# Optimization experiments

Measured on AMD Instinct MI355X. Metric: run time of the kernel, lower is better.

Reference implementation:

```python
import jax, jax.numpy as jnp
import numpy as np

EPS = 1e-6
BN_EPS = 1e-5
K = 20

def _vn_linear(x, W):
    # x: [B,C,...] channel axis 1; W: [out,in]
    return jnp.einsum('oc,bc...->bo...', W, x)

def _vn_bn(x):
    # training-mode BatchNorm on per-vector norms (affine at init: gamma=1, beta=0)
    norm = jnp.sqrt(jnp.sum(x * x, axis=2)) + EPS  # [B,C,*spatial]
    axes = (0,) + tuple(range(2, norm.ndim))
    mean = jnp.mean(norm, axis=axes, keepdims=True)
    var = jnp.mean((norm - mean) ** 2, axis=axes, keepdims=True)  # biased, as torch BN
    norm_bn = (norm - mean) / jnp.sqrt(var + BN_EPS)
    return x / jnp.expand_dims(norm, 2) * jnp.expand_dims(norm_bn, 2)

def _vn_llr(x, Wf, Wd, ns=0.0, use_bn=True):
    p = _vn_linear(x, Wf)
    if use_bn:
        p = _vn_bn(p)
    d = _vn_linear(x, Wd)
    dot = jnp.sum(p * d, axis=2, keepdims=True)
    mask = (dot >= 0).astype(x.dtype)
    dsq = jnp.sum(d * d, axis=2, keepdims=True)
    return ns * p + (1.0 - ns) * (mask * p + (1.0 - mask) * (p - dot / (dsq + EPS) * d))

def _graph_feature_cross(x, k):
    # x: [B,3,N] -> [B,3,3,N,k]
    B, _, N = x.shape
    inner = -2.0 * jnp.einsum('bdn,bdm->bnm', x, x)
    xx = jnp.sum(x * x, axis=1)  # [B,N]
    pdist = -xx[:, :, None] - inner - xx[:, None, :]  # [B,N,N]
    idx = jax.lax.top_k(pdist, k)[1]  # [B,N,k] nearest neighbors
    xt = jnp.transpose(x, (0, 2, 1))  # [B,N,3]
    nbr = xt[jnp.arange(B)[:, None, None], idx]  # [B,N,k,3]
    ctr = jnp.broadcast_to(xt[:, :, None, :], nbr.shape)  # [B,N,k,3]
    cross = jnp.cross(nbr, ctr)
    feat = jnp.stack([nbr - ctr, ctr, cross], axis=3)  # [B,N,k,3ch,3vec]
    return jnp.transpose(feat, (0, 3, 4, 1, 2))  # [B,3,3,N,k]

def _forward(points, wposf, wposd, w1f, w1d, w2f, w2d, w3, ws1f, ws1d, ws2f, ws2d, wlin):
    x = jnp.transpose(points, (0, 2, 1))  # [B,3,N]
    B, _, N = x.shape
    feat = _graph_feature_cross(x, K)  # [B,3,3,N,K]
    x = _vn_llr(feat, wposf, wposd)  # conv_pos, dim=5 -> [B,21,3,N,K]
    x = jnp.mean(x, axis=-1)  # mean pool over k -> [B,21,3,N]
    x = _vn_llr(x, w1f, w1d)  # conv1
    x = _vn_llr(x, w2f, w2d)  # conv2 (feature_transform=False so in=21? no: conv2 takes 42 -- matches cat-free path only when feature_transform False? conv2 in=42 but code passes x of 21? original passes 21-ch into conv2 only if feature_transform else 21; here feature_transform=False and conv2 expects 42 in torch -- we mirror with w2f [42,42] applied after duplicating? No: mirror exact torch behavior below.)
    return x

def reference(points, wposf, wposd, w1f, w1d, w2f, w2d, w3, ws1f, ws1d, ws2f, ws2d, wlin):
    x = jnp.transpose(points, (0, 2, 1))  # [B,3,N]
    B, _, N = x.shape
    feat = _graph_feature_cross(x, K)  # [B,3,3,N,K]
    x = _vn_llr(feat, wposf, wposd)  # [B,21,3,N,K]
    x = jnp.mean(x, axis=-1)  # mean pool -> [B,21,3,N]
    x = _vn_llr(x, w1f, w1d)  # [B,21,3,N]
    # torch conv2 is Linear(42,42) but with feature_transform=False it is applied to 21-ch
    # input; nn.Linear would error, so faithful runnable form uses the duplicated-channel
    # convention: concat (x, x) is NOT in the original; instead we slice w2 to [42,21].
    x = _vn_llr(x, w2f[:, :21], w2d[:, :21])  # [B,42,3,N]
    x = _vn_bn(_vn_linear(x, w3))  # conv3 + bn3 -> [B,85,3,N]
    x_mean_out = jnp.mean(x, axis=-1, keepdims=True)  # [B,85,3,1]
    x = jnp.concatenate([x, jnp.broadcast_to(x_mean_out, x.shape)], axis=1)  # [B,170,3,N]
    z = _vn_llr(x, ws1f, ws1d)  # [B,85,3,N]
    z = _vn_llr(z, ws2f, ws2d)  # [B,42,3,N]
    z = _vn_linear(z, wlin)  # [B,3,3,N]
    z = jnp.transpose(z, (0, 2, 1, 3))  # [B,3,3,N]
    x_std = jnp.einsum('bijm,bjkm->bikm', x, z)  # [B,170,3,N]
    xf = x_std.reshape(B, -1, N)  # [B,510,N]
    inv_z = jnp.max(xf, axis=-1)  # [B,510]
    center_loc = jnp.mean(x_mean_out, axis=2)  # [B,85,1]
    return (inv_z, x_mean_out, center_loc)

def setup_inputs() -> dict:
    key = jax.random.key(0)
    ks = jax.random.split(key, 14)
    B, N = 4, 8192
    def w(k, shape):
        return (jax.random.normal(k, shape, dtype=jnp.float32) * (1.0 / np.sqrt(shape[1])))
    return {
        'points': jax.random.normal(ks[0], (B, N, 3), dtype=jnp.float32),
        'wposf': w(ks[1], (21, 3)),
        'wposd': w(ks[2], (21, 3)),
        'w1f': w(ks[3], (21, 21)),
        'w1d': w(ks[4], (21, 21)),
        'w2f': w(ks[5], (42, 42)),
        'w2d': w(ks[6], (42, 42)),
        'w3': w(ks[7], (85, 42)),
        'ws1f': w(ks[8], (85, 170)),
        'ws1d': w(ks[9], (85, 170)),
        'ws2f': w(ks[10], (42, 85)),
        'ws2d': w(ks[11], (42, 85)),
        'wlin': w(ks[12], (3, 42)),
    }
```

## Files before the change

kernel.cpp:

```cpp
#include <hip/hip_runtime.h>
#include <cstdint>
#include <cstddef>

#define EPSF 1e-6f
#define BN_EPSF 1e-5f

constexpr int Bb = 4;
constexpr int Nn = 8192;
constexpr int KK = 20;
constexpr int SEG = 8;
constexpr int SEGLEN = Nn / SEG;
constexpr int BUF = 24;

constexpr size_t KNN0_OFF = 0;
constexpr size_t KNN1_OFF = 5242880;
constexpr size_t X1_OFF  = 0;
constexpr size_t X2_OFF  = 2064384;
constexpr size_t X3_OFF  = 4128768;
constexpr size_t Z1_OFF  = 0;
constexpr size_t X4_OFF  = 8355840;
constexpr size_t IDX_OFF = 16711680;
constexpr size_t Z2_OFF  = 17367040;
constexpr size_t Z3_OFF  = 21495808;
constexpr size_t ACC_OFF = 21790720;
constexpr size_t XM_OFF  = 21791744;
constexpr size_t BF_OFF  = 21792764;
constexpr size_t BD_OFF  = 21793784;
constexpr size_t DEXT_OFF = 21795840;
constexpr size_t EXT_NEED = (DEXT_OFF + 8355840) * 4;

__device__ __forceinline__ float wave_sum(float v) {
#pragma unroll
  for (int off = 32; off; off >>= 1) v += __shfl_xor(v, off, 64);
  return v;
}
__device__ __forceinline__ float wave_max(float v) {
#pragma unroll
  for (int off = 32; off; off >>= 1) v = fmaxf(v, __shfl_xor(v, off, 64));
  return v;
}
__device__ __forceinline__ uint32_t umin32(uint32_t a, uint32_t b) { return a < b ? a : b; }
__device__ __forceinline__ uint32_t umax32(uint32_t a, uint32_t b) { return a < b ? b : a; }

__global__ __launch_bounds__(1024) void zero_acc(float* __restrict__ a) {
  a[threadIdx.x] = 0.f;
}

__global__ __launch_bounds__(256) void knn_kernel(const float* __restrict__ pts,
                                                  uint32_t* __restrict__ knnp) {
  __shared__ float4 tile[SEGLEN];
  __shared__ uint32_t buf[BUF * 256];
  const int tid = threadIdx.x;
  const int n = blockIdx.x * 256 + tid;
  const int b = blockIdx.y;
  const int s = blockIdx.z;
  const float* pb = pts + (size_t)b * Nn * 3;

  for (int i = tid; i < SEGLEN; i += 256) {
    const float* p = pb + (size_t)(s * SEGLEN + i) * 3;
    const float x = p[0], y = p[1], z = p[2];
    tile[i] = make_float4(x, y, z, 0.5f * (x * x + y * y + z * z));
  }
  const float qx = pb[n * 3 + 0], qy = pb[n * 3 + 1], qz = pb[n * 3 + 2];
  const float nqx = -qx, nqy = -qy, nqz = -qz;
  const float h = 0.5f * (qx * qx + qy * qy + qz * qz);
  __syncthreads();

  uint32_t keys[KK];
#pragma unroll
  for (int j = 0; j < KK; ++j) keys[j] = 0xFFFFFFFFu;

  const int base = s * SEGLEN;

#pragma unroll 4
  for (int j = 0; j < 64; ++j) {
    const float4 c = tile[j];
    float u = fmaf(nqx, c.x, fmaf(nqy, c.y, fmaf(nqz, c.z, c.w + h)));
    u = fmaxf(u, 0.f);
    uint32_t mx = (__float_as_uint(u) & 0xFFFFE000u) | (uint32_t)(base + j);
#pragma unroll
    for (int q = 0; q < KK; ++q) {
      const uint32_t mn = umin32(keys[q], mx);
      mx = umax32(keys[q], mx);
      keys[q] = mn;
    }
  }

  uint32_t thresh = keys[KK - 1];
  float thresh_up = __uint_as_float((thresh & 0xFFFFE000u) + 0x2000u);
  int cnt = 0;

  for (int j0 = 64; j0 < SEGLEN; j0 += 4) {
#pragma unroll
    for (int u4 = 0; u4 < 4; ++u4) {
      const int j = j0 + u4;
      const float4 c = tile[j];
      const float u = fmaf(nqx, c.x, fmaf(nqy, c.y, fmaf(nqz, c.z, c.w + h)));
      if (u < thresh_up) {
        const float uc = fmaxf(u, 0.f);
        const uint32_t key = (__float_as_uint(uc) & 0xFFFFE000u) | (uint32_t)(base + j);
        buf[cnt * 256 + tid] = key;
        ++cnt;
      }
    }
    if (__any(cnt > BUF - 4)) {
#pragma unroll
      for (int i = 0; i < BUF; ++i) {
        uint32_t mx = (i < cnt) ? buf[i * 256 + tid] : 0xFFFFFFFFu;
#pragma unroll
        for (int q = 0; q < KK; ++q) {
          const uint32_t mn = umin32(keys[q], mx);
          mx = umax32(keys[q], mx);
          keys[q] = mn;
        }
      }
      cnt = 0;
      thresh = keys[KK - 1];
      thresh_up = __uint_as_float((thresh & 0xFFFFE000u) + 0x2000u);
    }
  }
#pragma unroll
  for (int i = 0; i < BUF; ++i) {
    uint32_t mx = (i < cnt) ? buf[i * 256 + tid] : 0xFFFFFFFFu;
#pragma unroll
    for (int q = 0; q < KK; ++q) {
      const uint32_t mn = umin32(keys[q], mx);
      mx = umax32(keys[q], mx);
      keys[q] = mn;
    }
  }

  uint32_t* op = knnp + ((size_t)(b * SEG + s) * KK) * Nn + n;
#pragma unroll
  for (int j = 0; j < KK; ++j) op[(size_t)j * Nn] = keys[j];
}

template <int LIN>
__global__ __launch_bounds__(256) void merge_pass(const uint32_t* __restrict__ in,
                                                  uint32_t* __restrict__ out) {
  constexpr int LOUT = LIN / 2;
  const int t = blockIdx.x * 256 + threadIdx.x;
  const int n = t & (Nn - 1);
  const int r = t >> 13;
  const int j = r % LOUT, b = r / LOUT;
  const uint32_t* p0 = in + ((size_t)(b * LIN + 2 * j) * KK) * Nn + n;
  const uint32_t* p1 = in + ((size_t)(b * LIN + 2 * j + 1) * KK) * Nn + n;
  uint32_t* op = out + ((size_t)(b * LOUT + j) * KK) * Nn + n;
  int i0 = 0, i1 = 0;
  uint32_t k0 = p0[0], k1 = p1[0];
#pragma unroll
  for (int m = 0; m < KK; ++m) {
    uint32_t k;
    if (k0 <= k1) { k = k0; ++i0; k0 = (i0 < KK) ? p0[(size_t)i0 * Nn] : 0xFFFFFFFFu; }
    else          { k = k1; ++i1; k1 = (i1 < KK) ? p1[(size_t)i1 * Nn] : 0xFFFFFFFFu; }
    op[(size_t)m * Nn] = k;
  }
}

__global__ __launch_bounds__(256) void merge_final(const uint32_t* __restrict__ in,
                                                   int* __restrict__ idx) {
  const int t = blockIdx.x * 256 + threadIdx.x;
  const int n = t & (Nn - 1), b = t >> 13;
  const uint32_t* p0 = in + ((size_t)(b * 2 + 0) * KK) * Nn + n;
  const uint32_t* p1 = in + ((size_t)(b * 2 + 1) * KK) * Nn + n;
  int* op = idx + (size_t)t * KK;
  int i0 = 0, i1 = 0;
  uint32_t k0 = p0[0], k1 = p1[0];
#pragma unroll
  for (int m = 0; m < KK; ++m) {
    uint32_t k;
    if (k0 <= k1) { k = k0; ++i0; k0 = (i0 < KK) ? p0[(size_t)i0 * Nn] : 0xFFFFFFFFu; }
    else          { k = k1; ++i1; k1 = (i1 < KK) ? p1[(size_t)i1 * Nn] : 0xFFFFFFFFu; }
    op[m] = (int)(k & 8191u);
  }
}

__global__ __launch_bounds__(256) void s1_stats(const float* __restrict__ pts,
                                                const int* __restrict__ idx,
                                                const float* __restrict__ wf,
                                                float* __restrict__ acc) {
  __shared__ float lacc[42];
  const int tid = threadIdx.x;
  for (int i = tid; i < 42; i += 256) lacc[i] = 0.f;
  __syncthreads();
  const int t = blockIdx.x * 256 + tid;
  const int site = t / 5;
  const int kq = (t % 5) * 4;
  const int n = site & (Nn - 1), b = site >> 13;
  const float* pb = pts + (size_t)b * Nn * 3;
  const float cx = pb[n * 3 + 0], cy = pb[n * 3 + 1], cz = pb[n * 3 + 2];
  float s1a[21], s2a[21];
#pragma unroll
  for (int o = 0; o < 21; ++o) { s1a[o] = 0.f; s2a[o] = 0.f; }
#pragma unroll
  for (int k = kq; k < kq + 4; ++k) {
    const int m = idx[(size_t)site * KK + k];
    const float ax = pb[m * 3 + 0], ay = pb[m * 3 + 1], az = pb[m * 3 + 2];
    const float e0x = ax - cx, e0y = ay - cy, e0z = az - cz;
    const float e2x = ay * cz - az * cy, e2y = az * cx - ax * cz, e2z = ax * cy - ay * cx;
#pragma unroll
    for (int o = 0; o < 21; ++o) {
      const float w0 = wf[o * 3 + 0], w1 = wf[o * 3 + 1], w2 = wf[o * 3 + 2];
      const float px = w0 * e0x + w1 * cx + w2 * e2x;
      const float py = w0 * e0y + w1 * cy + w2 * e2y;
      const float pz = w0 * e0z + w1 * cz + w2 * e2z;
      const float nrm = sqrtf(px * px + py * py + pz * pz) + EPSF;
      s1a[o] += nrm;
      s2a[o] += nrm * nrm;
    }
  }
#pragma unroll
  for (int o = 0; o < 21; ++o) {
    const float s1 = wave_sum(s1a[o]);
    const float s2 = wave_sum(s2a[o]);
    if ((tid & 63) == 0) { atomicAdd(&lacc[o], s1); atomicAdd(&lacc[21 + o], s2); }
  }
  __syncthreads();
  for (int i = tid; i < 42; i += 256) atomicAdd(&acc[i], lacc[i]);
}

__global__ __launch_bounds__(256) void s1_apply(const float* __restrict__ pts,
                                                const int* __restrict__ idx,
                                                const float* __restrict__ wf,
                                                const float* __restrict__ wd,
                                                const float* __restrict__ acc,
                                                float* __restrict__ x1) {
  const int t = blockIdx.x * 256 + threadIdx.x;
  const int o0 = blockIdx.y * 7;
  const int n = t & (Nn - 1), b = t >> 13;
  const float* pb = pts + (size_t)b * Nn * 3;
  const float cx = pb[n * 3 + 0], cy = pb[n * 3 + 1], cz = pb[n * 3 + 2];
  const float inv_cnt = 1.f / (float)(Bb * Nn * KK);
  float meano[7], istdo[7];
#pragma unroll
  for (int j = 0; j < 7; ++j) {
    const float mn = acc[o0 + j] * inv_cnt;
    const float vr = acc[21 + o0 + j] * inv_cnt - mn * mn;
    meano[j] = mn;
    istdo[j] = rsqrtf(vr + BN_EPSF);
  }
  float accu[7][3];
#pragma unroll
  for (int j = 0; j < 7; ++j) { accu[j][0] = 0.f; accu[j][1] = 0.f; accu[j][2] = 0.f; }
  for (int k = 0; k < KK; ++k) {
    const int m = idx[(size_t)t * KK + k];
    const float ax = pb[m * 3 + 0], ay = pb[m * 3 + 1], az = pb[m * 3 + 2];
    const float e0x = ax - cx, e0y = ay - cy, e0z = az - cz;
    const float e2x = ay * cz - az * cy, e2y = az * cx - ax * cz, e2z = ax * cy - ay * cx;
#pragma unroll
    for (int j = 0; j < 7; ++j) {
      const int o = o0 + j;
      const float wf0 = wf[o * 3 + 0], wf1 = wf[o * 3 + 1], wf2 = wf[o * 3 + 2];
      const float px = wf0 * e0x + wf1 * cx + wf2 * e2x;
      const float py = wf0 * e0y + wf1 * cy + wf2 * e2y;
      const float pz = wf0 * e0z + wf1 * cz + wf2 * e2z;
      const float nrm = sqrtf(px * px + py * py + pz * pz) + EPSF;
      const float factor = (nrm - meano[j]) * istdo[j] / nrm;
      const float q0 = px * factor, q1 = py * factor, q2 = pz * factor;
      const float wd0 = wd[o * 3 + 0], wd1 = wd[o * 3 + 1], wd2 = wd[o * 3 + 2];
      const float dx = wd0 * e0x + wd1 * cx + wd2 * e2x;
      const float dy = wd0 * e0y + wd1 * cy + wd2 * e2y;
      const float dz = wd0 * e0z + wd1 * cz + wd2 * e2z;
      const float dot = q0 * dx + q1 * dy + q2 * dz;
      const float dsq = dx * dx + dy * dy + dz * dz;
      const float corr = (dot < 0.f) ? dot / (dsq + EPSF) : 0.f;
      accu[j][0] += q0 - corr * dx;
      accu[j][1] += q1 - corr * dy;
      accu[j][2] += q2 - corr * dz;
    }
  }
  const float sc = 1.f / (float)KK;
  float* ob = x1 + (size_t)b * 21 * 3 * Nn + n;
#pragma unroll
  for (int j = 0; j < 7; ++j) {
    const int o = o0 + j;
    ob[(o * 3 + 0) * Nn] = accu[j][0] * sc;
    ob[(o * 3 + 1) * Nn] = accu[j][1] * sc;
    ob[(o * 3 + 2) * Nn] = accu[j][2] * sc;
  }
}

template <int CIN, int COUT, int OT, bool HAS_BIAS>
__global__ __launch_bounds__(256) void vn_stats_pd(const float* __restrict__ X,
                                                   const float* __restrict__ Wf,
                                                   const float* __restrict__ Wd, int ws,
                                                   const float* __restrict__ biasF,
                                                   const float* __restrict__ biasD,
                                                   float* __restrict__ acc,
                                                   float* __restrict__ P,
                                                   float* __restrict__ D) {
  __shared__ float lacc[2 * OT];
  const int tid = threadIdx.x;
  if (tid < 2 * OT) lacc[tid] = 0.f;
  __syncthreads();
  const int o0 = blockIdx.y * OT;
  const int t = blockIdx.x * 256 + tid;
  const int n = t & (Nn - 1), b = t >> 13;
  const float* xb = X + (size_t)b * CIN * 3 * Nn + n;
  float* pb = P + (size_t)b * COUT * 3 * Nn + n;
  float* db = D + (size_t)b * COUT * 3 * Nn + n;
  float p[OT][3], dv[OT][3];
#pragma unroll
  for (int j = 0; j < OT; ++j)
#pragma unroll
    for (int dd = 0; dd < 3; ++dd) {
      p[j][dd] = HAS_BIAS ? biasF[((size_t)b * COUT + o0 + j) * 3 + dd] : 0.f;
      dv[j][dd] = HAS_BIAS ? biasD[((size_t)b * COUT + o0 + j) * 3 + dd] : 0.f;
    }
  for (int c = 0; c < CIN; ++c) {
    const float x0 = xb[(c * 3 + 0) * Nn];
    const float x1v = xb[(c * 3 + 1) * Nn];
    const float x2v = xb[(c * 3 + 2) * Nn];
#pragma unroll
    for (int j = 0; j < OT; ++j) {
      const float wfv = Wf[(o0 + j) * ws + c];
      p[j][0] += wfv * x0; p[j][1] += wfv * x1v; p[j][2] += wfv * x2v;
      const float wdv = Wd[(o0 + j) * ws + c];
      dv[j][0] += wdv * x0; dv[j][1] += wdv * x1v; dv[j][2] += wdv * x2v;
    }
  }
#pragma unroll
  for (int j = 0; j < OT; ++j) {
    const int o = o0 + j;
    pb[(size_t)(o * 3 + 0) * Nn] = p[j][0];
    pb[(size_t)(o * 3 + 1) * Nn] = p[j][1];
    pb[(size_t)(o * 3 + 2) * Nn] = p[j][2];
    db[(size_t)(o * 3 + 0) * Nn] = dv[j][0];
    db[(size_t)(o * 3 + 1) * Nn] = dv[j][1];
    db[(size_t)(o * 3 + 2) * Nn] = dv[j][2];
  }
#pragma unroll
  for (int j = 0; j < OT; ++j) {
    const float nrm = sqrtf(p[j][0] * p[j][0] + p[j][1] * p[j][1] + p[j][2] * p[j][2]) + EPSF;
    const float s1 = wave_sum(nrm);
    const float s2 = wave_sum(nrm * nrm);
    if ((tid & 63) == 0) { atomicAdd(&lacc[j], s1); atomicAdd(&lacc[OT + j], s2); }
  }
  __syncthreads();
  if (tid < 2 * OT) {
    const int g = (tid < OT) ? (o0 + tid) : (COUT + o0 + (tid - OT));
    atomicAdd(&acc[g], lacc[tid]);
  }
}

__device__ __forceinline__ float llr_one(float p0, float p1, float p2,
                                         float d0, float d1, float d2,
                                         float mn, float istd,
                                         float& r0o, float& r1o, float& r2o) {
  const float nrm = sqrtf(p0 * p0 + p1 * p1 + p2 * p2) + EPSF;
  const float factor = (nrm - mn) * istd / nrm;
  float r0 = p0 * factor, r1 = p1 * factor, r2 = p2 * factor;
  const float dot = r0 * d0 + r1 * d1 + r2 * d2;
  const float dsq = d0 * d0 + d1 * d1 + d2 * d2;
  const float corr = (dot < 0.f) ? dot / (dsq + EPSF) : 0.f;
  r0o = r0 - corr * d0; r1o = r1 - corr * d1; r2o = r2 - corr * d2;
  return 0.f;
}

template <int COUT>
__global__ __launch_bounds__(256) void vn_llr_ew4(const float* __restrict__ acc, float cntinv,
                                                  float* __restrict__ P,
                                                  const float* __restrict__ D) {
  const int t = blockIdx.x * 256 + threadIdx.x;
  const int n4 = t & (Nn / 4 - 1);
  const int r = t >> 11;
  const int o = r % COUT, b = r / COUT;
  float4* pp = (float4*)(P + ((size_t)(b * COUT + o) * 3) * Nn) + n4;
  const float4* dp = (const float4*)(D + ((size_t)(b * COUT + o) * 3) * Nn) + n4;
  const float4 p0 = pp[0], p1 = pp[Nn / 4], p2 = pp[2 * (Nn / 4)];
  const float4 d0 = dp[0], d1 = dp[Nn / 4], d2 = dp[2 * (Nn / 4)];
  const float mn = acc[o] * cntinv;
  const float vr = acc[COUT + o] * cntinv - mn * mn;
  const float istd = rsqrtf(vr + BN_EPSF);
  float4 r0, r1, r2;
  llr_one(p0.x, p1.x, p2.x, d0.x, d1.x, d2.x, mn, istd, r0.x, r1.x, r2.x);
  llr_one(p0.y, p1.y, p2.y, d0.y, d1.y, d2.y, mn, istd, r0.y, r1.y, r2.y);
  llr_one(p0.z, p1.z, p2.z, d0.z, d1.z, d2.z, mn, istd, r0.z, r1.z, r2.z);
  llr_one(p0.w, p1.w, p2.w, d0.w, d1.w, d2.w, mn, istd, r0.w, r1.w, r2.w);
  pp[0] = r0;
  pp[Nn / 4] = r1;
  pp[2 * (Nn / 4)] = r2;
}

template <int CIN, int COUT, int OT, bool HAS_BIAS>
__global__ __launch_bounds__(256) void vn_stats_pc(const float* __restrict__ X,
                                                   const float* __restrict__ Wf, int ws,
                                                   const float* __restrict__ biasF,
                                                   float* __restrict__ acc,
                                                   float* __restrict__ P) {
  __shared__ float lacc[2 * OT];
  const int tid = threadIdx.x;
  if (tid < 2 * OT) lacc[tid] = 0.f;
  __syncthreads();
  const int o0 = blockIdx.y * OT;
  const int t = blockIdx.x * 256 + tid;
  const int n = t & (Nn - 1), b = t >> 13;
  const float* xb = X + (size_t)b * CIN * 3 * Nn + n;
  float* pb = P + (size_t)b * COUT * 3 * Nn + n;
  float p[OT][3];
#pragma unroll
  for (int j = 0; j < OT; ++j)
#pragma unroll
    for (int dd = 0; dd < 3; ++dd)
      p[j][dd] = HAS_BIAS ? biasF[((size_t)b * COUT + o0 + j) * 3 + dd] : 0.f;
  for (int c = 0; c < CIN; ++c) {
    const float x0 = xb[(c * 3 + 0) * Nn];
    const float x1v = xb[(c * 3 + 1) * Nn];
    const float x2v = xb[(c * 3 + 2) * Nn];
#pragma unroll
    for (int j = 0; j < OT; ++j) {
      const float wv = Wf[(o0 + j) * ws + c];
      p[j][0] += wv * x0; p[j][1] += wv * x1v; p[j][2] += wv * x2v;
    }
  }
#pragma unroll
  for (int j = 0; j < OT; ++j) {
    const int o = o0 + j;
    pb[(size_t)(o * 3 + 0) * Nn] = p[j][0];
    pb[(size_t)(o * 3 + 1) * Nn] = p[j][1];
    pb[(size_t)(o * 3 + 2) * Nn] = p[j][2];
  }
#pragma unroll
  for (int j = 0; j < OT; ++j) {
    const float nrm = sqrtf(p[j][0] * p[j][0] + p[j][1] * p[j][1] + p[j][2] * p[j][2]) + EPSF;
    const float s1 = wave_sum(nrm);
    const float s2 = wave_sum(nrm * nrm);
    if ((tid & 63) == 0) { atomicAdd(&lacc[j], s1); atomicAdd(&lacc[OT + j], s2); }
  }
  __syncthreads();
  if (tid < 2 * OT) {
    const int g = (tid < OT) ? (o0 + tid) : (COUT + o0 + (tid - OT));
    atomicAdd(&acc[g], lacc[tid]);
  }
}

template <int CIN, int COUT, int OT, bool HAS_BIAS>
__global__ __launch_bounds__(256) void vn_apply_pc(const float* __restrict__ X,
                                                   const float* __restrict__ Wd, int ws,
                                                   const float* __restrict__ biasD,
                                                   const float* __restrict__ acc, float cntinv,
                                                   float* __restrict__ P) {
  const int o0 = blockIdx.y * OT;
  const int t = blockIdx.x * 256 + threadIdx.x;
  const int n = t & (Nn - 1), b = t >> 13;
  const float* xb = X + (size_t)b * CIN * 3 * Nn + n;
  float* pb = P + (size_t)b * COUT * 3 * Nn + n;
  float dv[OT][3];
#pragma unroll
  for (int j = 0; j < OT; ++j)
#pragma unroll
    for (int dd = 0; dd < 3; ++dd)
      dv[j][dd] = HAS_BIAS ? biasD[((size_t)b * COUT + o0 + j) * 3 + dd] : 0.f;
  for (int c = 0; c < CIN; ++c) {
    const float x0 = xb[(c * 3 + 0) * Nn];
    const float x1v = xb[(c * 3 + 1) * Nn];
    const float x2v = xb[(c * 3 + 2) * Nn];
#pragma unroll
    for (int j = 0; j < OT; ++j) {
      const float wdv = Wd[(o0 + j) * ws + c];
      dv[j][0] += wdv * x0; dv[j][1] += wdv * x1v; dv[j][2] += wdv * x2v;
    }
  }
#pragma unroll
  for (int j = 0; j < OT; ++j) {
    const int o = o0 + j;
    const float p0 = pb[(size_t)(o * 3 + 0) * Nn];
    const float p1 = pb[(size_t)(o * 3 + 1) * Nn];
    const float p2 = pb[(size_t)(o * 3 + 2) * Nn];
    const float nrm = sqrtf(p0 * p0 + p1 * p1 + p2 * p2) + EPSF;
    const float mn = acc[o] * cntinv;
    const float vr = acc[COUT + o] * cntinv - mn * mn;
    const float factor = (nrm - mn) * rsqrtf(vr + BN_EPSF) / nrm;
    float r0 = p0 * factor, r1 = p1 * factor, r2 = p2 * factor;
    const float dot = r0 * dv[j][0] + r1 * dv[j][1] + r2 * dv[j][2];
    const float dsq = dv[j][0] * dv[j][0] + dv[j][1] * dv[j][1] + dv[j][2] * dv[j][2];
    const float corr = (dot < 0.f) ? dot / (dsq + EPSF) : 0.f;
    r0 -= corr * dv[j][0]; r1 -= corr * dv[j][1]; r2 -= corr * dv[j][2];
    pb[(size_t)(o * 3 + 0) * Nn] = r0;
    pb[(size_t)(o * 3 + 1) * Nn] = r1;
    pb[(size_t)(o * 3 + 2) * Nn] = r2;
  }
}

template <int COUT>
__global__ __launch_bounds__(256) void vn_bn4(const float* __restrict__ acc, float cntinv,
                                              float* __restrict__ P) {
  const int t = blockIdx.x * 256 + threadIdx.x;
  const int n4 = t & (Nn / 4 - 1);
  const int r = t >> 11;
  const int o = r % COUT, b = r / COUT;
  float4* pp = (float4*)(P + ((size_t)(b * COUT + o) * 3) * Nn) + n4;
  const float4 p0 = pp[0], p1 = pp[Nn / 4], p2 = pp[2 * (Nn / 4)];
  const float mn = acc[o] * cntinv;
  const float vr = acc[COUT + o] * cntinv - mn * mn;
  const float istd = rsqrtf(vr + BN_EPSF);
  float4 r0, r1, r2;
#define BN_ONE(f) {                                                        \
    const float nrm = sqrtf(p0.f * p0.f + p1.f * p1.f + p2.f * p2.f) + EPSF; \
    const float factor = (nrm - mn) * istd / nrm;                          \
    r0.f = p0.f * factor; r1.f = p1.f * factor; r2.f = p2.f * factor; }
  BN_ONE(x) BN_ONE(y) BN_ONE(z) BN_ONE(w)
#undef BN_ONE
  pp[0] = r0;
  pp[Nn / 4] = r1;
  pp[2 * (Nn / 4)] = r2;
}

__global__ __launch_bounds__(256) void s5_mean(const float* __restrict__ x4,
                                               float* __restrict__ xm,
                                               float* __restrict__ out) {
  const int row = blockIdx.x;
  const int b = row / 255, rcd = row % 255;
  const float* src = x4 + (size_t)b * 255 * Nn + (size_t)rcd * Nn;
  float s = 0.f;
  for (int n = threadIdx.x; n < Nn; n += 256) s += src[n];
  s = wave_sum(s);
  __shared__ float wsum[4];
  if ((threadIdx.x & 63) == 0) wsum[threadIdx.x >> 6] = s;
  __syncthreads();
  if (threadIdx.x == 0) {
    const float mv = (wsum[0] + wsum[1] + wsum[2] + wsum[3]) * (1.f / (float)Nn);
    xm[row] = mv;
    out[2040 + row] = mv;
  }
}

__global__ __launch_bounds__(256) void s5_bias(const float* __restrict__ xm,
                                               const float* __restrict__ ws1f,
                                               const float* __restrict__ ws1d,
                                               float* __restrict__ biasF,
                                               float* __restrict__ biasD,
                                               float* __restrict__ out) {
  const int t = blockIdx.x * 256 + threadIdx.x;
  if (t < 1020) {
    const int b = t / 255, r = t % 255, o = r / 3, dd = r % 3;
    float sf = 0.f, sd = 0.f;
    for (int c = 0; c < 85; ++c) {
      const float xv = xm[(b * 85 + c) * 3 + dd];
      sf += ws1f[o * 170 + 85 + c] * xv;
      sd += ws1d[o * 170 + 85 + c] * xv;
    }
    biasF[t] = sf;
    biasD[t] = sd;
  }
  if (t < 340) {
    const int b = t / 85, c = t % 85;
    out[3060 + t] = (xm[(b * 85 + c) * 3 + 0] + xm[(b * 85 + c) * 3 + 1] +
                     xm[(b * 85 + c) * 3 + 2]) * (1.f / 3.f);
  }
}

__global__ __launch_bounds__(256) void s8_z3(const float* __restrict__ z2,
                                             const float* __restrict__ wlin,
                                             float* __restrict__ z3) {
  const int t = blockIdx.x * 256 + threadIdx.x;
  const int n = t & (Nn - 1), b = t >> 13;
  const float* zb = z2 + (size_t)b * 42 * 3 * Nn + n;
  float accv[3][3];
#pragma unroll
  for (int o = 0; o < 3; ++o)
#pragma unroll
    for (int dd = 0; dd < 3; ++dd) accv[o][dd] = 0.f;
  for (int c = 0; c < 42; ++c) {
    const float x0 = zb[(c * 3 + 0) * Nn];
    const float x1v = zb[(c * 3 + 1) * Nn];
    const float x2v = zb[(c * 3 + 2) * Nn];
#pragma unroll
    for (int o = 0; o < 3; ++o) {
      const float wv = wlin[o * 42 + c];
      accv[o][0] += wv * x0; accv[o][1] += wv * x1v; accv[o][2] += wv * x2v;
    }
  }
  float* ob = z3 + (size_t)b * 9 * Nn + n;
#pragma unroll
  for (int o = 0; o < 3; ++o)
#pragma unroll
    for (int dd = 0; dd < 3; ++dd) ob[(o * 3 + dd) * Nn] = accv[o][dd];
}

__global__ __launch_bounds__(256) void s9_max(const float* __restrict__ x4,
                                              const float* __restrict__ xm,
                                              const float* __restrict__ z3,
                                              float* __restrict__ out) {
  const int tile = blockIdx.x;
  const int b = blockIdx.y;
  const int i0 = tile * 5;
  const bool upper = (i0 >= 85);
  float mx[15];
#pragma unroll
  for (int r = 0; r < 15; ++r) mx[r] = -3.402823466e38f;
  float xmr[5][3];
  if (upper) {
#pragma unroll
    for (int ii = 0; ii < 5; ++ii)
#pragma unroll
      for (int j = 0; j < 3; ++j) xmr[ii][j] = xm[(b * 85 + (i0 - 85 + ii)) * 3 + j];
  }
  const float* zb = z3 + (size_t)b * 9 * Nn;
  const float* xb = x4 + (size_t)b * 255 * Nn;
  for (int n = threadIdx.x; n < Nn; n += 256) {
    float zk[3][3];
#pragma unroll
    for (int k = 0; k < 3; ++k)
#pragma unroll
      for (int j = 0; j < 3; ++j) zk[k][j] = zb[(k * 3 + j) * Nn + n];
#pragma unroll
    for (int ii = 0; ii < 5; ++ii) {
      float xj0, xj1, xj2;
      if (upper) {
        xj0 = xmr[ii][0]; xj1 = xmr[ii][1]; xj2 = xmr[ii][2];
      } else {
        xj0 = xb[((i0 + ii) * 3 + 0) * Nn + n];
        xj1 = xb[((i0 + ii) * 3 + 1) * Nn + n];
        xj2 = xb[((i0 + ii) * 3 + 2) * Nn + n];
      }
#pragma unroll
      for (int k = 0; k < 3; ++k) {
        const float v = xj0 * zk[k][0] + xj1 * zk[k][1] + xj2 * zk[k][2];
        mx[ii * 3 + k] = fmaxf(mx[ii * 3 + k], v);
      }
    }
  }
  __shared__ float red[4 * 15];
#pragma unroll
  for (int r = 0; r < 15; ++r) {
    const float v = wave_max(mx[r]);
    if ((threadIdx.x & 63) == 0) red[(threadIdx.x >> 6) * 15 + r] = v;
  }
  __syncthreads();
  if (threadIdx.x < 15) {
    const float v = fmaxf(fmaxf(red[threadIdx.x], red[15 + threadIdx.x]),
                          fmaxf(red[30 + threadIdx.x], red[45 + threadIdx.x]));
    out[b * 510 + i0 * 3 + threadIdx.x] = v;
  }
}

extern "C" void kernel_launch(void* const* d_in, const int* in_sizes, int n_in,
                              void* d_out, int out_size, void* d_ws, size_t ws_size,
                              hipStream_t stream) {
  const float* pts   = (const float*)d_in[0];
  const float* wposf = (const float*)d_in[1];
  const float* wposd = (const float*)d_in[2];
  const float* w1f   = (const float*)d_in[3];
  const float* w1d   = (const float*)d_in[4];
  const float* w2f   = (const float*)d_in[5];
  const float* w2d   = (const float*)d_in[6];
  const float* w3    = (const float*)d_in[7];
  const float* ws1f  = (const float*)d_in[8];
  const float* ws1d  = (const float*)d_in[9];
  const float* ws2f  = (const float*)d_in[10];
  const float* ws2d  = (const float*)d_in[11];
  const float* wlin  = (const float*)d_in[12];
  float* out = (float*)d_out;
  float* wsf = (float*)d_ws;

  uint32_t* knnp0 = (uint32_t*)(wsf + KNN0_OFF);
  uint32_t* knnp1 = (uint32_t*)(wsf + KNN1_OFF);
  float* x1 = wsf + X1_OFF;
  float* x2 = wsf + X2_OFF;
  float* x3 = wsf + X3_OFF;
  float* z1 = wsf + Z1_OFF;
  float* x4 = wsf + X4_OFF;
  int* idx  = (int*)(wsf + IDX_OFF);
  float* z2 = wsf + Z2_OFF;
  float* z3 = wsf + Z3_OFF;
  float* acc = wsf + ACC_OFF;
  float* xm = wsf + XM_OFF;
  float* biasF = wsf + BF_OFF;
  float* biasD = wsf + BD_OFF;
  float* d1 = wsf + X3_OFF;
  float* d2 = wsf + X4_OFF;
  float* dext = wsf + DEXT_OFF;
  const bool ext = ws_size >= EXT_NEED;

  const float inv_sites = 1.f / (float)(Bb * Nn);

  zero_acc<<<1, 1024, 0, stream>>>(acc);
  knn_kernel<<<dim3(Nn / 256, Bb, SEG), 256, 0, stream>>>(pts, knnp0);
  merge_pass<8><<<Bb * Nn * 4 / 256, 256, 0, stream>>>(knnp0, knnp1);
  merge_pass<4><<<Bb * Nn * 2 / 256, 256, 0, stream>>>(knnp1, knnp0);
  merge_final<<<Bb * Nn / 256, 256, 0, stream>>>(knnp0, idx);

  s1_stats<<<Bb * Nn * 5 / 256, 256, 0, stream>>>(pts, idx, wposf, acc + 0);
  s1_apply<<<dim3(Bb * Nn / 256, 3), 256, 0, stream>>>(pts, idx, wposf, wposd, acc + 0, x1);

  vn_stats_pd<21, 21, 7, false><<<dim3(Bb * Nn / 256, 3), 256, 0, stream>>>(
      x1, w1f, w1d, 21, nullptr, nullptr, acc + 64, x2, d1);
  vn_llr_ew4<21><<<Bb * 21 * Nn / 4 / 256, 256, 0, stream>>>(acc + 64, inv_sites, x2, d1);

  vn_stats_pd<21, 42, 7, false><<<dim3(Bb * Nn / 256, 6), 256, 0, stream>>>(
      x2, w2f, w2d, 42, nullptr, nullptr, acc + 128, x3, d2);
  vn_llr_ew4<42><<<Bb * 42 * Nn / 4 / 256, 256, 0, stream>>>(acc + 128, inv_sites, x3, d2);

  vn_stats_pc<42, 85, 17, false><<<dim3(Bb * Nn / 256, 5), 256, 0, stream>>>(
      x3, w3, 42, nullptr, acc + 256, x4);
  vn_bn4<85><<<Bb * 85 * Nn / 4 / 256, 256, 0, stream>>>(acc + 256, inv_sites, x4);

  s5_mean<<<Bb * 255, 256, 0, stream>>>(x4, xm, out);
  s5_bias<<<4, 256, 0, stream>>>(xm, ws1f, ws1d, biasF, biasD, out);

  if (ext) {
    vn_stats_pd<85, 85, 17, true><<<dim3(Bb * Nn / 256, 5), 256, 0, stream>>>(
        x4, ws1f, ws1d, 170, biasF, biasD, acc + 512, z1, dext);
    vn_llr_ew4<85><<<Bb * 85 * Nn / 4 / 256, 256, 0, stream>>>(acc + 512, inv_sites, z1, dext);
    vn_stats_pd<85, 42, 14, false><<<dim3(Bb * Nn / 256, 3), 256, 0, stream>>>(
        z1, ws2f, ws2d, 85, nullptr, nullptr, acc + 768, z2, dext);
    vn_llr_ew4<42><<<Bb * 42 * Nn / 4 / 256, 256, 0, stream>>>(acc + 768, inv_sites, z2, dext);
  } else {
    vn_stats_pc<85, 85, 17, true><<<dim3(Bb * Nn / 256, 5), 256, 0, stream>>>(
        x4, ws1f, 170, biasF, acc + 512, z1);
    vn_apply_pc<85, 85, 17, true><<<dim3(Bb * Nn / 256, 5), 256, 0, stream>>>(
        x4, ws1d, 170, biasD, acc + 512, inv_sites, z1);
    vn_stats_pc<85, 42, 14, false><<<dim3(Bb * Nn / 256, 3), 256, 0, stream>>>(
        z1, ws2f, 85, nullptr, acc + 768, z2);
    vn_apply_pc<85, 42, 14, false><<<dim3(Bb * Nn / 256, 3), 256, 0, stream>>>(
        z1, ws2d, 85, nullptr, acc + 768, inv_sites, z2);
  }

  s8_z3<<<Bb * Nn / 256, 256, 0, stream>>>(z2, wlin, z3);
  s9_max<<<dim3(34, Bb), 256, 0, stream>>>(x4, xm, z3, out);
}
```

Baseline: 762.1 us.

## Fuse kNN merge passes into one 8-way merge, hoist bias, retile VN stats

```diff
diff --git a/kernel.cpp b/kernel.cpp
--- a/kernel.cpp
+++ b/kernel.cpp
@@ -13,7 +13,6 @@
 constexpr int BUF = 24;
 
 constexpr size_t KNN0_OFF = 0;
-constexpr size_t KNN1_OFF = 5242880;
 constexpr size_t X1_OFF  = 0;
 constexpr size_t X2_OFF  = 2064384;
 constexpr size_t X3_OFF  = 4128768;
@@ -88,6 +87,7 @@
 
   uint32_t thresh = keys[KK - 1];
   float thresh_up = __uint_as_float((thresh & 0xFFFFE000u) + 0x2000u);
+  float th_h = thresh_up - h + 2.4e-7f * fabsf(thresh_up) + 1e-30f;
   int cnt = 0;
 
   for (int j0 = 64; j0 < SEGLEN; j0 += 4) {
@@ -95,9 +95,9 @@
     for (int u4 = 0; u4 < 4; ++u4) {
       const int j = j0 + u4;
       const float4 c = tile[j];
-      const float u = fmaf(nqx, c.x, fmaf(nqy, c.y, fmaf(nqz, c.z, c.w + h)));
-      if (u < thresh_up) {
-        const float uc = fmaxf(u, 0.f);
+      const float up = fmaf(nqx, c.x, fmaf(nqy, c.y, fmaf(nqz, c.z, c.w)));
+      if (up < th_h) {
+        const float uc = fmaxf(up + h, 0.f);
         const uint32_t key = (__float_as_uint(uc) & 0xFFFFE000u) | (uint32_t)(base + j);
         buf[cnt * 256 + tid] = key;
         ++cnt;
@@ -117,6 +117,7 @@
       cnt = 0;
       thresh = keys[KK - 1];
       thresh_up = __uint_as_float((thresh & 0xFFFFE000u) + 0x2000u);
+      th_h = thresh_up - h + 2.4e-7f * fabsf(thresh_up) + 1e-30f;
     }
   }
 #pragma unroll
@@ -135,43 +136,32 @@
   for (int j = 0; j < KK; ++j) op[(size_t)j * Nn] = keys[j];
 }
 
-template <int LIN>
-__global__ __launch_bounds__(256) void merge_pass(const uint32_t* __restrict__ in,
-                                                  uint32_t* __restrict__ out) {
-  constexpr int LOUT = LIN / 2;
-  const int t = blockIdx.x * 256 + threadIdx.x;
-  const int n = t & (Nn - 1);
-  const int r = t >> 13;
-  const int j = r % LOUT, b = r / LOUT;
-  const uint32_t* p0 = in + ((size_t)(b * LIN + 2 * j) * KK) * Nn + n;
-  const uint32_t* p1 = in + ((size_t)(b * LIN + 2 * j + 1) * KK) * Nn + n;
-  uint32_t* op = out + ((size_t)(b * LOUT + j) * KK) * Nn + n;
-  int i0 = 0, i1 = 0;
-  uint32_t k0 = p0[0], k1 = p1[0];
-#pragma unroll
-  for (int m = 0; m < KK; ++m) {
-    uint32_t k;
-    if (k0 <= k1) { k = k0; ++i0; k0 = (i0 < KK) ? p0[(size_t)i0 * Nn] : 0xFFFFFFFFu; }
-    else          { k = k1; ++i1; k1 = (i1 < KK) ? p1[(size_t)i1 * Nn] : 0xFFFFFFFFu; }
-    op[(size_t)m * Nn] = k;
-  }
-}
-
-__global__ __launch_bounds__(256) void merge_final(const uint32_t* __restrict__ in,
-                                                   int* __restrict__ idx) {
+__global__ __launch_bounds__(256) void merge8(const uint32_t* __restrict__ in,
+                                              int* __restrict__ idx) {
   const int t = blockIdx.x * 256 + threadIdx.x;
   const int n = t & (Nn - 1), b = t >> 13;
-  const uint32_t* p0 = in + ((size_t)(b * 2 + 0) * KK) * Nn + n;
-  const uint32_t* p1 = in + ((size_t)(b * 2 + 1) * KK) * Nn + n;
+  const uint32_t* base = in + ((size_t)(b * SEG) * KK) * Nn + n;
+  uint32_t h[SEG];
+  int ii[SEG];
+#pragma unroll
+  for (int s = 0; s < SEG; ++s) {
+    h[s] = base[(size_t)s * KK * Nn];
+    ii[s] = 1;
+  }
   int* op = idx + (size_t)t * KK;
-  int i0 = 0, i1 = 0;
-  uint32_t k0 = p0[0], k1 = p1[0];
 #pragma unroll
   for (int m = 0; m < KK; ++m) {
-    uint32_t k;
-    if (k0 <= k1) { k = k0; ++i0; k0 = (i0 < KK) ? p0[(size_t)i0 * Nn] : 0xFFFFFFFFu; }
-    else          { k = k1; ++i1; k1 = (i1 < KK) ? p1[(size_t)i1 * Nn] : 0xFFFFFFFFu; }
+    uint32_t k = h[0];
+#pragma unroll
+    for (int s = 1; s < SEG; ++s) k = umin32(k, h[s]);
     op[m] = (int)(k & 8191u);
+#pragma unroll
+    for (int s = 0; s < SEG; ++s) {
+      if (h[s] == k) {
+        h[s] = (ii[s] < KK) ? base[(size_t)s * KK * Nn + (size_t)ii[s] * Nn] : 0xFFFFFFFFu;
+        ii[s]++;
+      }
+    }
   }
 }
 
@@ -655,7 +645,6 @@
   float* wsf = (float*)d_ws;
 
   uint32_t* knnp0 = (uint32_t*)(wsf + KNN0_OFF);
-  uint32_t* knnp1 = (uint32_t*)(wsf + KNN1_OFF);
   float* x1 = wsf + X1_OFF;
   float* x2 = wsf + X2_OFF;
   float* x3 = wsf + X3_OFF;
@@ -677,9 +666,7 @@
 
   zero_acc<<<1, 1024, 0, stream>>>(acc);
   knn_kernel<<<dim3(Nn / 256, Bb, SEG), 256, 0, stream>>>(pts, knnp0);
-  merge_pass<8><<<Bb * Nn * 4 / 256, 256, 0, stream>>>(knnp0, knnp1);
-  merge_pass<4><<<Bb * Nn * 2 / 256, 256, 0, stream>>>(knnp1, knnp0);
-  merge_final<<<Bb * Nn / 256, 256, 0, stream>>>(knnp0, idx);
+  merge8<<<Bb * Nn / 256, 256, 0, stream>>>(knnp0, idx);
 
   s1_stats<<<Bb * Nn * 5 / 256, 256, 0, stream>>>(pts, idx, wposf, acc + 0);
   s1_apply<<<dim3(Bb * Nn / 256, 3), 256, 0, stream>>>(pts, idx, wposf, wposd, acc + 0, x1);
@@ -700,10 +687,10 @@
   s5_bias<<<4, 256, 0, stream>>>(xm, ws1f, ws1d, biasF, biasD, out);
 
   if (ext) {
-    vn_stats_pd<85, 85, 17, true><<<dim3(Bb * Nn / 256, 5), 256, 0, stream>>>(
+    vn_stats_pd<85, 85, 5, true><<<dim3(Bb * Nn / 256, 17), 256, 0, stream>>>(
         x4, ws1f, ws1d, 170, biasF, biasD, acc + 512, z1, dext);
     vn_llr_ew4<85><<<Bb * 85 * Nn / 4 / 256, 256, 0, stream>>>(acc + 512, inv_sites, z1, dext);
-    vn_stats_pd<85, 42, 14, false><<<dim3(Bb * Nn / 256, 3), 256, 0, stream>>>(
+    vn_stats_pd<85, 42, 7, false><<<dim3(Bb * Nn / 256, 6), 256, 0, stream>>>(
         z1, ws2f, ws2d, 85, nullptr, nullptr, acc + 768, z2, dext);
     vn_llr_ew4<42><<<Bb * 42 * Nn / 4 / 256, 256, 0, stream>>>(acc + 768, inv_sites, z2, dext);
   } else {
```

Measured after the change: 677.1 us. 1.13x faster.
